# Kernel tuning notes

Hardware: AMD Instinct MI355X
Metric: run time of the kernel (lower is better)

The kernel has to match this reference:

```python
import jax, jax.numpy as jnp
import numpy as np

HIDDEN = 2048
N_HEADS = 32
N_KV = 4
HEAD_DIM = 128
EPS = 1e-6
THETA = 1e6
B, S = 2, 2048


def setup_inputs() -> dict:
    key = jax.random.key(0)
    k1, k2, k3 = jax.random.split(key, 3)
    hidden_states = jax.random.normal(k1, (B, S, HIDDEN), dtype=jnp.float32)
    positions = jnp.broadcast_to(jnp.arange(S, dtype=jnp.int32), (B, S))
    w_qkv = jax.random.normal(k2, ((N_HEADS + 2 * N_KV) * HEAD_DIM, HIDDEN), dtype=jnp.float32) * 0.02
    w_o = jax.random.normal(k3, (HIDDEN, N_HEADS * HEAD_DIM), dtype=jnp.float32) * 0.02
    q_norm_w = jnp.ones((HEAD_DIM,), dtype=jnp.float32)
    k_norm_w = jnp.ones((HEAD_DIM,), dtype=jnp.float32)
    return {"hidden_states": hidden_states, "positions": positions,
            "w_qkv": w_qkv, "w_o": w_o, "q_norm_w": q_norm_w, "k_norm_w": k_norm_w}


def _rms_norm(x, w):
    # x: [..., HEAD_DIM]
    var = jnp.mean(x * x, axis=-1, keepdims=True)
    return x * jax.lax.rsqrt(var + EPS) * w


def _rope(x, positions):
    # NEOX-style rotary. x: [B,S,H,D], positions: [B,S]
    half = HEAD_DIM // 2
    inv_freq = 1.0 / (THETA ** (jnp.arange(0, half, dtype=jnp.float32) / half))
    ang = positions.astype(jnp.float32)[..., None] * inv_freq  # [B,S,half]
    cos = jnp.cos(ang)[:, :, None, :]
    sin = jnp.sin(ang)[:, :, None, :]
    x1, x2 = x[..., :half], x[..., half:]
    return jnp.concatenate([x1 * cos - x2 * sin, x2 * cos + x1 * sin], axis=-1)


def reference(hidden_states, positions, w_qkv, w_o, q_norm_w, k_norm_w):
    q_size = N_HEADS * HEAD_DIM
    kv_size = N_KV * HEAD_DIM
    qkv = jnp.einsum('bsh,oh->bso', hidden_states, w_qkv)
    q = qkv[..., :q_size].reshape(B, S, N_HEADS, HEAD_DIM)
    k = qkv[..., q_size:q_size + kv_size].reshape(B, S, N_KV, HEAD_DIM)
    v = qkv[..., q_size + kv_size:].reshape(B, S, N_KV, HEAD_DIM)
    # per-head RMSNorm then RoPE
    q = _rope(_rms_norm(q, q_norm_w), positions)
    k = _rope(_rms_norm(k, k_norm_w), positions)
    rep = N_HEADS // N_KV
    k = jnp.repeat(k, rep, axis=2)
    v = jnp.repeat(v, rep, axis=2)
    scale = HEAD_DIM ** -0.5
    scores = jnp.einsum('bqhd,bkhd->bhqk', q, k) * scale
    causal = jnp.tril(jnp.ones((S, S), dtype=bool))
    scores = jnp.where(causal, scores, jnp.finfo(scores.dtype).min)
    probs = jax.nn.softmax(scores, axis=-1)
    attn = jnp.einsum('bhqk,bkhd->bqhd', probs, v).reshape(B, S, N_HEADS * HEAD_DIM)
    return jnp.einsum('bsa,ha->bsh', attn, w_o)
```

## Files before the change

### kernel.cpp

```cpp
#include <hip/hip_runtime.h>
#include <cstdint>

#define SEQ 2048
#define BATCH 2
#define NTOK 4096
#define HID 2048
#define NH 32
#define NKV 4
#define HD 128
#define QKV_O 5120

typedef __attribute__((ext_vector_type(8))) short short8;
typedef __attribute__((ext_vector_type(8))) unsigned short u16x8;
typedef __attribute__((ext_vector_type(4))) unsigned short u16x4;
typedef __attribute__((ext_vector_type(4))) float f32x4;

__device__ __forceinline__ float bf2f(unsigned short u) {
  union { unsigned int i; float f; } v; v.i = ((unsigned int)u) << 16; return v.f;
}
__device__ __forceinline__ unsigned short f2bf(float f) {
  union { float f; unsigned int i; } v; v.f = f;
  unsigned int r = v.i + 0x7FFFu + ((v.i >> 16) & 1u);
  return (unsigned short)(r >> 16);
}

__device__ __forceinline__ void load_lds16(const void* g, void* l) {
  __builtin_amdgcn_global_load_lds((const __attribute__((address_space(1))) unsigned int*)g,
                                   (__attribute__((address_space(3))) unsigned int*)l, 16, 0, 0);
}

__global__ __launch_bounds__(256) void convert_to_bf16(const float* __restrict__ src,
                                                       unsigned short* __restrict__ dst,
                                                       int n4) {
  int i = blockIdx.x * blockDim.x + threadIdx.x;
  int stride = gridDim.x * blockDim.x;
  for (; i < n4; i += stride) {
    f32x4 v = *(const f32x4*)(src + 4 * (size_t)i);
    u16x4 o;
    o.x = f2bf(v.x); o.y = f2bf(v.y); o.z = f2bf(v.z); o.w = f2bf(v.w);
    *(u16x4*)(dst + 4 * (size_t)i) = o;
  }
}

template <bool OUT_F32>
__global__ __launch_bounds__(256) void gemm_bt_bf16(
    const unsigned short* __restrict__ A, const unsigned short* __restrict__ B,
    void* __restrict__ Cv, int lda, int ldb, int ldc, int K) {
  __shared__ alignas(16) unsigned short As[128 * 32];
  __shared__ alignas(16) unsigned short Bs[128 * 32];

  const int t    = threadIdx.x;
  const int lane = t & 63;
  const int w    = t >> 6;
  const int wm   = (w >> 1) * 64;
  const int wn   = (w & 1) * 64;
  const size_t m0 = (size_t)blockIdx.y * 128;
  const size_t n0 = (size_t)blockIdx.x * 128;

  f32x4 acc[4][4] = {};

  const int srow = w * 32 + (lane >> 2);
  const int scol = (lane & 3) * 8;
  const unsigned short* gA0 = &A[(m0 + srow) * (size_t)lda + scol];
  const unsigned short* gA1 = gA0 + 16 * (size_t)lda;
  const unsigned short* gB0 = &B[(n0 + srow) * (size_t)ldb + scol];
  const unsigned short* gB1 = gB0 + 16 * (size_t)ldb;
  unsigned short* lA0 = &As[(w * 32) * 32];
  unsigned short* lA1 = &As[(w * 32 + 16) * 32];
  unsigned short* lB0 = &Bs[(w * 32) * 32];
  unsigned short* lB1 = &Bs[(w * 32 + 16) * 32];

  const int fr = lane & 15;
  const int kb = (lane >> 4) * 8;

  for (int k0 = 0; k0 < K; k0 += 32) {
    load_lds16(gA0 + k0, lA0);
    load_lds16(gA1 + k0, lA1);
    load_lds16(gB0 + k0, lB0);
    load_lds16(gB1 + k0, lB1);
    __syncthreads();
    short8 af[4], bf[4];
#pragma unroll
    for (int mt = 0; mt < 4; mt++) af[mt] = *(const short8*)&As[(wm + mt * 16 + fr) * 32 + kb];
#pragma unroll
    for (int nt = 0; nt < 4; nt++) bf[nt] = *(const short8*)&Bs[(wn + nt * 16 + fr) * 32 + kb];
#pragma unroll
    for (int mt = 0; mt < 4; mt++)
#pragma unroll
      for (int nt = 0; nt < 4; nt++)
        acc[mt][nt] = __builtin_amdgcn_mfma_f32_16x16x32_bf16(af[mt], bf[nt], acc[mt][nt], 0, 0, 0);
    __syncthreads();
  }

  const int r4 = (lane >> 4) * 4;
  const int cc = lane & 15;
#pragma unroll
  for (int mt = 0; mt < 4; mt++)
#pragma unroll
    for (int nt = 0; nt < 4; nt++) {
      size_t row = m0 + wm + mt * 16 + r4;
      size_t col = n0 + wn + nt * 16 + cc;
#pragma unroll
      for (int r = 0; r < 4; r++) {
        if (OUT_F32) ((float*)Cv)[(row + r) * ldc + col] = acc[mt][nt][r];
        else ((unsigned short*)Cv)[(row + r) * ldc + col] = f2bf(acc[mt][nt][r]);
      }
    }
}

__global__ __launch_bounds__(64) void rope_tab(const int* __restrict__ pos,
                                               float2* __restrict__ tab) {
  const int tok = blockIdx.x;
  const int j = threadIdx.x;
  float p = (float)pos[tok];
  float inv_freq = expf((float)j * (-13.815510557964274f / 64.0f));
  float ang = p * inv_freq;
  float2 cs; cs.x = cosf(ang); cs.y = sinf(ang);
  tab[tok * 64 + j] = cs;
}

__global__ __launch_bounds__(256) void normrope(
    unsigned short* __restrict__ qkv, const float2* __restrict__ tab,
    const unsigned short* __restrict__ qw, const unsigned short* __restrict__ kw) {
  const int wv   = threadIdx.x >> 6;
  const int lane = threadIdx.x & 63;
  const int h    = blockIdx.x * 4 + wv;
  const int tok  = blockIdx.z * SEQ + blockIdx.y;

  const unsigned short* w = (h < NH) ? qw : kw;
  const size_t src = (size_t)tok * QKV_O + (size_t)h * HD;

  float x1 = bf2f(qkv[src + lane]);
  float x2 = bf2f(qkv[src + lane + 64]);
  float ss = x1 * x1 + x2 * x2;
#pragma unroll
  for (int off = 32; off; off >>= 1) ss += __shfl_xor(ss, off);
  float r = rsqrtf(ss * (1.0f / 128.0f) + 1e-6f);
  float n1 = x1 * r * bf2f(w[lane]);
  float n2 = x2 * r * bf2f(w[lane + 64]);

  float2 cs = tab[tok * 64 + lane];
  qkv[src + lane]      = f2bf(n1 * cs.x - n2 * cs.y);
  qkv[src + lane + 64] = f2bf(n2 * cs.x + n1 * cs.y);
}

__global__ __launch_bounds__(256) void transpose_v(const unsigned short* __restrict__ qkv,
                                                   unsigned short* __restrict__ vt) {
  __shared__ alignas(16) unsigned short Vs[64][136];
  const int k0 = blockIdx.x * 64, kvh = blockIdx.y, b = blockIdx.z;
  const int t = threadIdx.x;
  const int voff = (NH + NKV) * HD + kvh * HD;
  {
    const int row = t >> 2, cb = (t & 3) * 8;
    const size_t gb = (size_t)(b * SEQ + k0 + row) * QKV_O + voff;
#pragma unroll
    for (int r = 0; r < 4; r++)
      *(uint4*)&Vs[row][cb + 32 * r] = *(const uint4*)&qkv[gb + cb + 32 * r];
  }
  __syncthreads();
  const int d = t >> 1, half = t & 1;
  const size_t ob = ((size_t)((b * NKV + kvh) * HD + d)) * SEQ + k0 + half * 32;
#pragma unroll
  for (int i = 0; i < 4; i++) {
    u16x8 vv;
#pragma unroll
    for (int j = 0; j < 8; j++) vv[j] = Vs[half * 32 + i * 8 + j][d];
    *(u16x8*)&vt[ob + i * 8] = vv;
  }
}

__global__ __launch_bounds__(512, 4) void flash_mfma(unsigned short* __restrict__ qkv,
                                                     const unsigned short* __restrict__ vt) {
  __shared__ alignas(16) unsigned short Kbuf[2][64 * 128];
  __shared__ alignas(16) unsigned short Vbuf[2][128 * 64];
  __shared__ alignas(16) unsigned short Ps[8][16 * 64];

  const int p = (int)blockIdx.x;
  const int h = blockIdx.y, b = blockIdx.z;
  const int t = threadIdx.x;
  const int lane = t & 63, w = t >> 6;
  const int c = lane & 15, g = lane >> 4;
  const int kvh = h >> 3;
  const int koff = NH * HD + kvh * HD;
  const float scale = 0.08838834764831845f;
  const int swz = c & 7;
  const int nqt = SEQ / 128;

  const int rK0 = t >> 4,         jK0 = (t & 15) ^ (rK0 & 15);
  const int rK1 = (t + 512) >> 4, jK1 = ((t + 512) & 15) ^ (rK1 & 15);
  const int dV0 = t >> 3,         jV0 = (t & 7) ^ (dV0 & 7);
  const int dV1 = (t + 512) >> 3, jV1 = ((t + 512) & 7) ^ (dV1 & 7);
  const unsigned short* gK0 = qkv + (size_t)(b * SEQ + rK0) * QKV_O + koff + jK0 * 8;
  const unsigned short* gK1 = qkv + (size_t)(b * SEQ + rK1) * QKV_O + koff + jK1 * 8;
  const unsigned short* gV0 = vt + ((size_t)(b * NKV + kvh) * HD + dV0) * SEQ + jV0 * 8;
  const unsigned short* gV1 = vt + ((size_t)(b * NKV + kvh) * HD + dV1) * SEQ + jV1 * 8;

  auto stage = [&](int k0s, int bi) {
    load_lds16(gK0 + (size_t)k0s * QKV_O, &Kbuf[bi][(w * 64) * 8]);
    load_lds16(gK1 + (size_t)k0s * QKV_O, &Kbuf[bi][(w * 64 + 512) * 8]);
    load_lds16(gV0 + k0s, &Vbuf[bi][(w * 64) * 8]);
    load_lds16(gV1 + k0s, &Vbuf[bi][(w * 64 + 512) * 8]);
  };

  for (int job = 0; job < 2; job++) {
    const int qt = job == 0 ? (nqt - 1 - p) : p;
    const int q0 = qt * 128;
    const int nkt = 2 * qt + 2;

    stage(0, 0);

    short8 qf[4];
    {
      const size_t qr = (size_t)(b * SEQ + q0 + w * 16 + c) * QKV_O + (size_t)h * HD;
#pragma unroll
      for (int ks = 0; ks < 4; ks++)
        qf[ks] = *(const short8*)&qkv[qr + ks * 32 + g * 8];
    }

    f32x4 O[8] = {};
    float m_i = -1e30f, l_i = 0.0f;

    for (int kt = 0; kt < nkt; kt++) {
      const int cur = kt & 1;
      asm volatile("s_waitcnt vmcnt(0)" ::: "memory");
      __builtin_amdgcn_s_barrier();
      __builtin_amdgcn_sched_barrier(0);
      if (kt + 1 < nkt) stage((kt + 1) * 64, cur ^ 1);

      const unsigned short* Kc = Kbuf[cur];
      const unsigned short* Vc = Vbuf[cur];

      f32x4 sc[4];
#pragma unroll
      for (int mt = 0; mt < 4; mt++) sc[mt] = (f32x4){0.f, 0.f, 0.f, 0.f};
      __builtin_amdgcn_s_setprio(1);
#pragma unroll
      for (int ks = 0; ks < 4; ks++) {
#pragma unroll
        for (int mt = 0; mt < 4; mt++) {
          short8 kf = *(const short8*)&Kc[(mt * 16 + c) * 128 + (((ks * 4 + g) ^ c) * 8)];
          sc[mt] = __builtin_amdgcn_mfma_f32_16x16x32_bf16(kf, qf[ks], sc[mt], 0, 0, 0);
        }
      }
      __builtin_amdgcn_s_setprio(0);

      const int k0 = kt * 64;
      const int qrow = q0 + w * 16 + c;
      const bool need_mask = (k0 + 63 > q0 + w * 16);
      float mx = -3.0e38f;
#pragma unroll
      for (int mt = 0; mt < 4; mt++)
#pragma unroll
        for (int r = 0; r < 4; r++) {
          float s = sc[mt][r];
          if (need_mask && (k0 + mt * 16 + g * 4 + r > qrow)) s = -3.0e38f;
          sc[mt][r] = s;
          mx = fmaxf(mx, s);
        }
      mx = fmaxf(mx, __shfl_xor(mx, 16));
      mx = fmaxf(mx, __shfl_xor(mx, 32));
      float mxs = mx * scale;

      if (!__all(mxs - m_i <= 8.0f)) {
        float m_new = fmaxf(m_i, mxs);
        float alpha = __expf(m_i - m_new);
        f32x4 a4;
#pragma unroll
        for (int r = 0; r < 4; r++) a4[r] = __shfl(alpha, g * 4 + r);
#pragma unroll
        for (int nt = 0; nt < 8; nt++)
#pragma unroll
          for (int r = 0; r < 4; r++) O[nt][r] *= a4[r];
        l_i *= alpha;
        m_i = m_new;
      }

      float psum = 0.0f;
#pragma unroll
      for (int mt = 0; mt < 4; mt++) {
        u16x4 p4;
#pragma unroll
        for (int r = 0; r < 4; r++) {
          float pv = __expf(__builtin_fmaf(sc[mt][r], scale, -m_i));
          psum += pv;
          p4[r] = f2bf(pv);
        }
        *(u16x4*)&Ps[w][c * 64 + (((mt * 2 + (g >> 1)) ^ swz) * 8) + (g & 1) * 4] = p4;
      }
      psum += __shfl_xor(psum, 16);
      psum += __shfl_xor(psum, 32);
      l_i += psum;

      __builtin_amdgcn_s_setprio(1);
#pragma unroll
      for (int ks = 0; ks < 2; ks++) {
        short8 pf = *(const short8*)&Ps[w][c * 64 + (((ks * 4 + g) ^ swz) * 8)];
#pragma unroll
        for (int nt = 0; nt < 8; nt++) {
          short8 vf = *(const short8*)&Vc[(nt * 16 + c) * 64 + (((ks * 4 + g) ^ swz) * 8)];
          O[nt] = __builtin_amdgcn_mfma_f32_16x16x32_bf16(pf, vf, O[nt], 0, 0, 0);
        }
      }
      __builtin_amdgcn_s_setprio(0);
    }

    f32x4 l4;
#pragma unroll
    for (int r = 0; r < 4; r++) l4[r] = __shfl(l_i, g * 4 + r);
    f32x4 li;
#pragma unroll
    for (int r = 0; r < 4; r++) li[r] = 1.0f / l4[r];
#pragma unroll
    for (int nt = 0; nt < 8; nt++)
#pragma unroll
      for (int r = 0; r < 4; r++) {
        size_t addr = (size_t)(b * SEQ + q0 + w * 16 + g * 4 + r) * QKV_O + h * HD + nt * 16 + c;
        qkv[addr] = f2bf(O[nt][r] * li[r]);
      }
  }
}

extern "C" void kernel_launch(void* const* d_in, const int* in_sizes, int n_in,
                              void* d_out, int out_size, void* d_ws, size_t ws_size,
                              hipStream_t stream) {
  const float* hidden_f = (const float*)d_in[0];
  const int* positions  = (const int*)d_in[1];
  const float* wqkv_f   = (const float*)d_in[2];
  const float* wo_f     = (const float*)d_in[3];
  const float* qn_f     = (const float*)d_in[4];
  const float* kn_f     = (const float*)d_in[5];
  float* out            = (float*)d_out;

  char* ws = (char*)d_ws;
  unsigned short* hidden_c = (unsigned short*)ws;
  unsigned short* wqkv_c   = (unsigned short*)(ws + 16777216);
  unsigned short* wo_c     = (unsigned short*)(ws + 37748736);
  unsigned short* qn_c     = (unsigned short*)(ws + 54525952);
  unsigned short* kn_c     = (unsigned short*)(ws + 54526208);
  unsigned short* qkv      = (unsigned short*)(ws + 54526464);
  unsigned short* vt_g     = (unsigned short*)(ws + 96469504);
  float2* rtab             = (float2*)ws;

  convert_to_bf16<<<1024, 256, 0, stream>>>(hidden_f, hidden_c, NTOK * HID / 4);
  convert_to_bf16<<<1024, 256, 0, stream>>>(wqkv_f, wqkv_c, QKV_O * HID / 4);
  convert_to_bf16<<<1024, 256, 0, stream>>>(wo_f, wo_c, HID * NH * HD / 4);
  convert_to_bf16<<<1, 32, 0, stream>>>(qn_f, qn_c, HD / 4);
  convert_to_bf16<<<1, 32, 0, stream>>>(kn_f, kn_c, HD / 4);

  gemm_bt_bf16<false><<<dim3(QKV_O / 128, NTOK / 128), 256, 0, stream>>>(
      hidden_c, wqkv_c, qkv, HID, HID, QKV_O, HID);
  rope_tab<<<NTOK, 64, 0, stream>>>(positions, rtab);
  normrope<<<dim3((NH + NKV) / 4, SEQ, BATCH), 256, 0, stream>>>(qkv, rtab, qn_c, kn_c);
  transpose_v<<<dim3(SEQ / 64, NKV, BATCH), 256, 0, stream>>>(qkv, vt_g);
  flash_mfma<<<dim3(SEQ / 256, NH, BATCH), 512, 0, stream>>>(qkv, vt_g);
  gemm_bt_bf16<true><<<dim3(HID / 128, NTOK / 128), 256, 0, stream>>>(
      qkv, wo_c, out, QKV_O, NH * HD, HID, NH * HD);
}
```

Baseline: 505.0 us.

## Use 256x256 double-buffered swizzled GEMM with split-K for output projection

Measured after the change: 480.0 us. -5.0%, faster.

```diff
diff --git a/kernel.cpp b/kernel.cpp
--- a/kernel.cpp
+++ b/kernel.cpp
@@ -42,68 +42,100 @@
   }
 }
 
-template <bool OUT_F32>
-__global__ __launch_bounds__(256) void gemm_bt_bf16(
+__global__ __launch_bounds__(256) void reduce_add(float* __restrict__ out,
+                                                  const float* __restrict__ part, int n4) {
+  int i = blockIdx.x * blockDim.x + threadIdx.x;
+  int stride = gridDim.x * blockDim.x;
+  for (; i < n4; i += stride) {
+    f32x4 a = *(const f32x4*)(out + 4 * (size_t)i);
+    f32x4 b = *(const f32x4*)(part + 4 * (size_t)i);
+    a.x += b.x; a.y += b.y; a.z += b.z; a.w += b.w;
+    *(f32x4*)(out + 4 * (size_t)i) = a;
+  }
+}
+
+template <bool OUT_F32, bool SPLIT>
+__global__ __launch_bounds__(512, 2) void gemm256(
     const unsigned short* __restrict__ A, const unsigned short* __restrict__ B,
-    void* __restrict__ Cv, int lda, int ldb, int ldc, int K) {
-  __shared__ alignas(16) unsigned short As[128 * 32];
-  __shared__ alignas(16) unsigned short Bs[128 * 32];
-
-  const int t    = threadIdx.x;
-  const int lane = t & 63;
-  const int w    = t >> 6;
-  const int wm   = (w >> 1) * 64;
-  const int wn   = (w & 1) * 64;
-  const size_t m0 = (size_t)blockIdx.y * 128;
-  const size_t n0 = (size_t)blockIdx.x * 128;
-
-  f32x4 acc[4][4] = {};
-
-  const int srow = w * 32 + (lane >> 2);
-  const int scol = (lane & 3) * 8;
-  const unsigned short* gA0 = &A[(m0 + srow) * (size_t)lda + scol];
-  const unsigned short* gA1 = gA0 + 16 * (size_t)lda;
-  const unsigned short* gB0 = &B[(n0 + srow) * (size_t)ldb + scol];
-  const unsigned short* gB1 = gB0 + 16 * (size_t)ldb;
-  unsigned short* lA0 = &As[(w * 32) * 32];
-  unsigned short* lA1 = &As[(w * 32 + 16) * 32];
-  unsigned short* lB0 = &Bs[(w * 32) * 32];
-  unsigned short* lB1 = &Bs[(w * 32 + 16) * 32];
-
-  const int fr = lane & 15;
-  const int kb = (lane >> 4) * 8;
-
-  for (int k0 = 0; k0 < K; k0 += 32) {
-    load_lds16(gA0 + k0, lA0);
-    load_lds16(gA1 + k0, lA1);
-    load_lds16(gB0 + k0, lB0);
-    load_lds16(gB1 + k0, lB1);
-    __syncthreads();
-    short8 af[4], bf[4];
-#pragma unroll
-    for (int mt = 0; mt < 4; mt++) af[mt] = *(const short8*)&As[(wm + mt * 16 + fr) * 32 + kb];
-#pragma unroll
-    for (int nt = 0; nt < 4; nt++) bf[nt] = *(const short8*)&Bs[(wn + nt * 16 + fr) * 32 + kb];
-#pragma unroll
-    for (int mt = 0; mt < 4; mt++)
-#pragma unroll
-      for (int nt = 0; nt < 4; nt++)
-        acc[mt][nt] = __builtin_amdgcn_mfma_f32_16x16x32_bf16(af[mt], bf[nt], acc[mt][nt], 0, 0, 0);
-    __syncthreads();
-  }
-
-  const int r4 = (lane >> 4) * 4;
-  const int cc = lane & 15;
-#pragma unroll
-  for (int mt = 0; mt < 4; mt++)
-#pragma unroll
-    for (int nt = 0; nt < 4; nt++) {
-      size_t row = m0 + wm + mt * 16 + r4;
-      size_t col = n0 + wn + nt * 16 + cc;
+    void* __restrict__ C0, void* __restrict__ C1,
+    int lda, int ldb, int ldc, int Kloop) {
+  __shared__ alignas(16) unsigned short As[2][256 * 64];
+  __shared__ alignas(16) unsigned short Bs[2][256 * 64];
+
+  const int t = threadIdx.x;
+  const int lane = t & 63, w = t >> 6;
+  const int fr = lane & 15, g = lane >> 4;
+  const int wm = w >> 2, wn = w & 3;
+  const size_t m0 = (size_t)blockIdx.y * 256;
+  const size_t n0 = (size_t)blockIdx.x * 256;
+  const int kbase = SPLIT ? (int)blockIdx.z * Kloop : 0;
+  void* Cv = (SPLIT && blockIdx.z) ? C1 : C0;
+
+  const int srow = w * 8 + (lane >> 3);
+  const int sch = (lane & 7) ^ ((lane >> 3) & 7);
+  const unsigned short* gA[4];
+  const unsigned short* gB[4];
+#pragma unroll
+  for (int i = 0; i < 4; i++) {
+    gA[i] = A + (m0 + i * 64 + srow) * (size_t)lda + kbase + sch * 8;
+    gB[i] = B + (n0 + i * 64 + srow) * (size_t)ldb + kbase + sch * 8;
+  }
+
+  auto stage = [&](int k0, int bi) {
+#pragma unroll
+    for (int i = 0; i < 4; i++) {
+      load_lds16(gA[i] + k0, &As[bi][(i * 512 + w * 64) * 8]);
+      load_lds16(gB[i] + k0, &Bs[bi][(i * 512 + w * 64) * 8]);
+    }
+  };
+
+  f32x4 acc[8][4] = {};
+  stage(0, 0);
+
+  const int nk = Kloop / 64;
+  for (int kt = 0; kt < nk; kt++) {
+    const int cur = kt & 1;
+    asm volatile("s_waitcnt vmcnt(0)" ::: "memory");
+    __builtin_amdgcn_s_barrier();
+    __builtin_amdgcn_sched_barrier(0);
+    if (kt + 1 < nk) stage((kt + 1) * 64, cur ^ 1);
+
+    const unsigned short* Ac = As[cur];
+    const unsigned short* Bc = Bs[cur];
+
+    short8 bfr[4][2];
+#pragma unroll
+    for (int nf = 0; nf < 4; nf++) {
+      const int row = wn * 64 + nf * 16 + fr;
+#pragma unroll
+      for (int s = 0; s < 2; s++)
+        bfr[nf][s] = *(const short8*)&Bc[row * 64 + (((s * 4 + g) ^ (fr & 7)) * 8)];
+    }
+    __builtin_amdgcn_s_setprio(1);
+#pragma unroll
+    for (int mf = 0; mf < 8; mf++) {
+      const int row = wm * 128 + mf * 16 + fr;
+      short8 af0 = *(const short8*)&Ac[row * 64 + (((0 + g) ^ (fr & 7)) * 8)];
+      short8 af1 = *(const short8*)&Ac[row * 64 + (((4 + g) ^ (fr & 7)) * 8)];
+#pragma unroll
+      for (int nf = 0; nf < 4; nf++) {
+        acc[mf][nf] = __builtin_amdgcn_mfma_f32_16x16x32_bf16(af0, bfr[nf][0], acc[mf][nf], 0, 0, 0);
+        acc[mf][nf] = __builtin_amdgcn_mfma_f32_16x16x32_bf16(af1, bfr[nf][1], acc[mf][nf], 0, 0, 0);
+      }
+    }
+    __builtin_amdgcn_s_setprio(0);
+  }
+
+#pragma unroll
+  for (int mf = 0; mf < 8; mf++)
+#pragma unroll
+    for (int nf = 0; nf < 4; nf++) {
+      size_t row = m0 + wm * 128 + mf * 16 + g * 4;
+      size_t col = n0 + wn * 64 + nf * 16 + fr;
 #pragma unroll
       for (int r = 0; r < 4; r++) {
-        if (OUT_F32) ((float*)Cv)[(row + r) * ldc + col] = acc[mt][nt][r];
-        else ((unsigned short*)Cv)[(row + r) * ldc + col] = f2bf(acc[mt][nt][r]);
+        if (OUT_F32) ((float*)Cv)[(row + r) * ldc + col] = acc[mf][nf][r];
+        else ((unsigned short*)Cv)[(row + r) * ldc + col] = f2bf(acc[mf][nf][r]);
       }
     }
 }
@@ -340,6 +372,7 @@
   unsigned short* qkv      = (unsigned short*)(ws + 54526464);
   unsigned short* vt_g     = (unsigned short*)(ws + 96469504);
   float2* rtab             = (float2*)ws;
+  float* p0                = (float*)ws;
 
   convert_to_bf16<<<1024, 256, 0, stream>>>(hidden_f, hidden_c, NTOK * HID / 4);
   convert_to_bf16<<<1024, 256, 0, stream>>>(wqkv_f, wqkv_c, QKV_O * HID / 4);
@@ -347,12 +380,13 @@
   convert_to_bf16<<<1, 32, 0, stream>>>(qn_f, qn_c, HD / 4);
   convert_to_bf16<<<1, 32, 0, stream>>>(kn_f, kn_c, HD / 4);
 
-  gemm_bt_bf16<false><<<dim3(QKV_O / 128, NTOK / 128), 256, 0, stream>>>(
-      hidden_c, wqkv_c, qkv, HID, HID, QKV_O, HID);
+  gemm256<false, false><<<dim3(QKV_O / 256, NTOK / 256), 512, 0, stream>>>(
+      hidden_c, wqkv_c, qkv, qkv, HID, HID, QKV_O, HID);
   rope_tab<<<NTOK, 64, 0, stream>>>(positions, rtab);
   normrope<<<dim3((NH + NKV) / 4, SEQ, BATCH), 256, 0, stream>>>(qkv, rtab, qn_c, kn_c);
   transpose_v<<<dim3(SEQ / 64, NKV, BATCH), 256, 0, stream>>>(qkv, vt_g);
   flash_mfma<<<dim3(SEQ / 256, NH, BATCH), 512, 0, stream>>>(qkv, vt_g);
-  gemm_bt_bf16<true><<<dim3(HID / 128, NTOK / 128), 256, 0, stream>>>(
-      qkv, wo_c, out, QKV_O, NH * HD, HID, NH * HD);
-}
+  gemm256<true, true><<<dim3(HID / 256, NTOK / 256, 2), 512, 0, stream>>>(
+      qkv, wo_c, p0, out, QKV_O, NH * HD, HID, NH * HD / 2);
+  reduce_add<<<2048, 256, 0, stream>>>(out, p0, NTOK * HID / 4);
+}
```

## Add 256x256 four-stage pipelined GEMM and split-K for output projection

Applied to the files above, without the earlier changes.

After: 513.2 us. About the same (+1.6%).

```diff
diff --git a/kernel.cpp b/kernel.cpp
--- a/kernel.cpp
+++ b/kernel.cpp
@@ -42,6 +42,111 @@
   }
 }
 
+__global__ __launch_bounds__(256) void reduce_add(float* __restrict__ out,
+                                                  const float* __restrict__ part, int n4) {
+  int i = blockIdx.x * blockDim.x + threadIdx.x;
+  int stride = gridDim.x * blockDim.x;
+  for (; i < n4; i += stride) {
+    f32x4 a = *(const f32x4*)(out + 4 * (size_t)i);
+    f32x4 b = *(const f32x4*)(part + 4 * (size_t)i);
+    a.x += b.x; a.y += b.y; a.z += b.z; a.w += b.w;
+    *(f32x4*)(out + 4 * (size_t)i) = a;
+  }
+}
+
+template <bool OUT_F32, bool SPLIT>
+__global__ __launch_bounds__(512, 2) void gemm256_p4(
+    const unsigned short* __restrict__ A, const unsigned short* __restrict__ B,
+    void* __restrict__ C0, void* __restrict__ C1,
+    int lda, int ldb, int ldc, int Kloop) {
+  __shared__ alignas(16) unsigned short As[4][256 * 32];
+  __shared__ alignas(16) unsigned short Bs[4][256 * 32];
+
+  const int t = threadIdx.x;
+  const int lane = t & 63, w = t >> 6;
+  const int fr = lane & 15, g = lane >> 4;
+  const int wm = w >> 2, wn = w & 3;
+  const size_t m0 = (size_t)blockIdx.y * 256;
+  const size_t n0 = (size_t)blockIdx.x * 256;
+  const int kbase = SPLIT ? (int)blockIdx.z * Kloop : 0;
+  void* Cv = (SPLIT && blockIdx.z) ? C1 : C0;
+
+  const int rA0 = t >> 2;         const int cA0 = (t & 3) ^ (rA0 & 3);
+  const int rA1 = (t + 512) >> 2; const int cA1 = ((t + 512) & 3) ^ (rA1 & 3);
+  const unsigned short* gA0 = A + (m0 + rA0) * (size_t)lda + kbase + cA0 * 8;
+  const unsigned short* gA1 = A + (m0 + rA1) * (size_t)lda + kbase + cA1 * 8;
+  const unsigned short* gB0 = B + (n0 + rA0) * (size_t)ldb + kbase + cA0 * 8;
+  const unsigned short* gB1 = B + (n0 + rA1) * (size_t)ldb + kbase + cA1 * 8;
+
+  auto stage = [&](int s) {
+    const int bi = s & 3;
+    const int kk = s * 32;
+    load_lds16(gA0 + kk, &As[bi][(w * 64) * 8]);
+    load_lds16(gA1 + kk, &As[bi][(512 + w * 64) * 8]);
+    load_lds16(gB0 + kk, &Bs[bi][(w * 64) * 8]);
+    load_lds16(gB1 + kk, &Bs[bi][(512 + w * 64) * 8]);
+  };
+
+  f32x4 acc[8][4] = {};
+  const int NK = Kloop / 32;
+  stage(0); stage(1); stage(2);
+
+  const int kc = (g ^ (fr & 3)) * 8;
+  const int arow = wm * 128 + fr;
+  const int brow = wn * 64 + fr;
+
+  for (int s = 0; s < NK; s++) {
+    asm volatile("s_waitcnt vmcnt(8)" ::: "memory");
+    __builtin_amdgcn_s_barrier();
+    __builtin_amdgcn_sched_barrier(0);
+    if (s + 3 < NK) stage(s + 3);
+
+    const unsigned short* Ac = As[s & 3];
+    const unsigned short* Bc = Bs[s & 3];
+
+    short8 bfr[4];
+#pragma unroll
+    for (int nf = 0; nf < 4; nf++)
+      bfr[nf] = *(const short8*)&Bc[(brow + nf * 16) * 32 + kc];
+    short8 af[4];
+#pragma unroll
+    for (int mf = 0; mf < 4; mf++)
+      af[mf] = *(const short8*)&Ac[(arow + mf * 16) * 32 + kc];
+    __builtin_amdgcn_s_setprio(1);
+#pragma unroll
+    for (int mf = 0; mf < 4; mf++)
+#pragma unroll
+      for (int nf = 0; nf < 4; nf++)
+        acc[mf][nf] = __builtin_amdgcn_mfma_f32_16x16x32_bf16(af[mf], bfr[nf], acc[mf][nf], 0, 0, 0);
+    __builtin_amdgcn_s_setprio(0);
+
+    short8 af2[4];
+#pragma unroll
+    for (int mf = 0; mf < 4; mf++)
+      af2[mf] = *(const short8*)&Ac[(arow + (mf + 4) * 16) * 32 + kc];
+    __builtin_amdgcn_s_setprio(1);
+#pragma unroll
+    for (int mf = 0; mf < 4; mf++)
+#pragma unroll
+      for (int nf = 0; nf < 4; nf++)
+        acc[mf + 4][nf] = __builtin_amdgcn_mfma_f32_16x16x32_bf16(af2[mf], bfr[nf], acc[mf + 4][nf], 0, 0, 0);
+    __builtin_amdgcn_s_setprio(0);
+  }
+
+#pragma unroll
+  for (int mf = 0; mf < 8; mf++)
+#pragma unroll
+    for (int nf = 0; nf < 4; nf++) {
+      size_t row = m0 + wm * 128 + mf * 16 + g * 4;
+      size_t col = n0 + wn * 64 + nf * 16 + fr;
+#pragma unroll
+      for (int r = 0; r < 4; r++) {
+        if (OUT_F32) ((float*)Cv)[(row + r) * ldc + col] = acc[mf][nf][r];
+        else ((unsigned short*)Cv)[(row + r) * ldc + col] = f2bf(acc[mf][nf][r]);
+      }
+    }
+}
+
 template <bool OUT_F32>
 __global__ __launch_bounds__(256) void gemm_bt_bf16(
     const unsigned short* __restrict__ A, const unsigned short* __restrict__ B,
@@ -340,6 +445,7 @@
   unsigned short* qkv      = (unsigned short*)(ws + 54526464);
   unsigned short* vt_g     = (unsigned short*)(ws + 96469504);
   float2* rtab             = (float2*)ws;
+  float* p0                = (float*)ws;
 
   convert_to_bf16<<<1024, 256, 0, stream>>>(hidden_f, hidden_c, NTOK * HID / 4);
   convert_to_bf16<<<1024, 256, 0, stream>>>(wqkv_f, wqkv_c, QKV_O * HID / 4);
@@ -347,12 +453,15 @@
   convert_to_bf16<<<1, 32, 0, stream>>>(qn_f, qn_c, HD / 4);
   convert_to_bf16<<<1, 32, 0, stream>>>(kn_f, kn_c, HD / 4);
 
-  gemm_bt_bf16<false><<<dim3(QKV_O / 128, NTOK / 128), 256, 0, stream>>>(
-      hidden_c, wqkv_c, qkv, HID, HID, QKV_O, HID);
+  gemm256_p4<false, false><<<dim3(NH * HD / 256, NTOK / 256), 512, 0, stream>>>(
+      hidden_c, wqkv_c, qkv, qkv, HID, HID, QKV_O, HID);
+  gemm_bt_bf16<false><<<dim3(2 * NKV * HD / 128, NTOK / 128), 256, 0, stream>>>(
+      hidden_c, wqkv_c + (size_t)(NH * HD) * HID, qkv + NH * HD, HID, HID, QKV_O, HID);
   rope_tab<<<NTOK, 64, 0, stream>>>(positions, rtab);
   normrope<<<dim3((NH + NKV) / 4, SEQ, BATCH), 256, 0, stream>>>(qkv, rtab, qn_c, kn_c);
   transpose_v<<<dim3(SEQ / 64, NKV, BATCH), 256, 0, stream>>>(qkv, vt_g);
   flash_mfma<<<dim3(SEQ / 256, NH, BATCH), 512, 0, stream>>>(qkv, vt_g);
-  gemm_bt_bf16<true><<<dim3(HID / 128, NTOK / 128), 256, 0, stream>>>(
-      qkv, wo_c, out, QKV_O, NH * HD, HID, NH * HD);
-}
+  gemm256_p4<true, true><<<dim3(HID / 256, NTOK / 256, 2), 512, 0, stream>>>(
+      qkv, wo_c, p0, out, QKV_O, NH * HD, HID, NH * HD / 2);
+  reduce_add<<<2048, 256, 0, stream>>>(out, p0, NTOK * HID / 4);
+}
```
